# Performance work log

Measured on AMD Instinct MI355X. Metric: run time of the kernel, lower is better.

Reference implementation:

```python
import jax, jax.numpy as jnp
import numpy as np


def _layernorm(x, g, b, eps=1e-5):
    mu = jnp.mean(x, axis=-1, keepdims=True)
    xc = x - mu
    var = jnp.mean(xc * xc, axis=-1, keepdims=True)
    return xc * jax.lax.rsqrt(var + eps) * g + b


def _s5(u, Lambda_re, Lambda_im, B_re, B_im, C_re, C_im, Dskip, log_step):
    # Diagonal complex SSM with ZOH discretization (S5).
    Lam = Lambda_re + 1j * Lambda_im                       # (P,) complex64
    Lam_bar = jnp.exp(Lam * jnp.exp(log_step))             # (P,)
    B_bar = ((Lam_bar - 1.0) / Lam)[:, None] * (B_re + 1j * B_im)  # (P, D)
    Bu = jnp.einsum('bld,pd->blp', u.astype(jnp.complex64), B_bar)  # (B, L, P)
    A = jnp.broadcast_to(Lam_bar, Bu.shape)

    def combine(e1, e2):
        a1, b1 = e1
        a2, b2 = e2
        return a1 * a2, a2 * b1 + b2

    _, xs = jax.lax.associative_scan(combine, (A, Bu), axis=1)  # parallel scan over L
    y = 2.0 * jnp.real(jnp.einsum('blp,dp->bld', xs, C_re + 1j * C_im))
    return y + Dskip * u


def setup_inputs() -> dict:
    key = jax.random.key(0)
    ks = jax.random.split(key, 10)
    B, L, D, P = 4, 2048, 1024, 64
    F = int(D * 2.0)  # ff_mult = 2.0
    x = jax.random.normal(ks[0], (B, L, D), jnp.float32)
    ln1_g = jnp.ones((D,), jnp.float32)
    ln1_b = jnp.zeros((D,), jnp.float32)
    ln2_g = jnp.ones((D,), jnp.float32)
    ln2_b = jnp.zeros((D,), jnp.float32)
    Lambda_re = -(0.5 + jax.random.uniform(ks[1], (P,), jnp.float32))  # stable poles
    Lambda_im = jnp.pi * jnp.arange(P, dtype=jnp.float32)              # HiPPO-like spread
    B_re = jax.random.normal(ks[2], (P, D), jnp.float32) / np.float32(np.sqrt(D))
    B_im = jax.random.normal(ks[3], (P, D), jnp.float32) / np.float32(np.sqrt(D))
    C_re = jax.random.normal(ks[4], (D, P), jnp.float32) / np.float32(np.sqrt(P))
    C_im = jax.random.normal(ks[5], (D, P), jnp.float32) / np.float32(np.sqrt(P))
    Dskip = jax.random.normal(ks[6], (D,), jnp.float32)
    dt_min, dt_max = 1e-3, 1e-1
    log_step = (np.float32(np.log(dt_min))
                + jax.random.uniform(ks[7], (P,), jnp.float32)
                * np.float32(np.log(dt_max) - np.log(dt_min)))
    W_enc = jax.random.normal(ks[8], (2 * F, D), jnp.float32) / np.float32(np.sqrt(D))
    W_dec = jax.random.normal(ks[9], (D, F), jnp.float32) / np.float32(np.sqrt(F))
    return dict(x=x, ln1_g=ln1_g, ln1_b=ln1_b, ln2_g=ln2_g, ln2_b=ln2_b,
                Lambda_re=Lambda_re, Lambda_im=Lambda_im, B_re=B_re, B_im=B_im,
                C_re=C_re, C_im=C_im, Dskip=Dskip, log_step=log_step,
                W_enc=W_enc, W_dec=W_dec)


def reference(x, ln1_g, ln1_b, ln2_g, ln2_b, Lambda_re, Lambda_im, B_re, B_im,
              C_re, C_im, Dskip, log_step, W_enc, W_dec):
    # S5Block: pre-LN -> S5 -> GELU -> residual (dropout = identity in eval)
    fx = _layernorm(x, ln1_g, ln1_b)
    h = jax.nn.gelu(_s5(fx, Lambda_re, Lambda_im, B_re, B_im, C_re, C_im, Dskip, log_step),
                    approximate=False) + fx
    # pre-LN GEGLU feed-forward -> residual
    fx2 = _layernorm(h, ln2_g, ln2_b)
    e = fx2 @ W_enc.T                      # (B, L, 2F)
    a, gate = jnp.split(e, 2, axis=-1)
    e = a * jax.nn.gelu(gate, approximate=False)
    return e @ W_dec.T + fx2
```

## Files before the change

### kernel.cpp

```cpp
#include <hip/hip_runtime.h>
#include <hip/hip_bf16.h>
#include <math.h>

typedef unsigned short u16;
typedef __bf16 v8bf __attribute__((ext_vector_type(8)));
typedef float f32x4 __attribute__((ext_vector_type(4)));
typedef float f32x16 __attribute__((ext_vector_type(16)));

__device__ __forceinline__ float us2f(u16 h) {
    union { unsigned int u; float f; } v; v.u = ((unsigned int)h) << 16; return v.f;
}
__device__ __forceinline__ u16 f2us(float f) {
    union { float f; unsigned int u; } v; v.f = f;
    unsigned int r = v.u + 0x7fffu + ((v.u >> 16) & 1u);
    return (u16)(r >> 16);
}
__device__ __forceinline__ float gelu_f(float x) {
    return 0.5f * x * (1.0f + erff(x * 0.70710678118654752f));
}
__device__ __forceinline__ void gload_lds16(const u16* g, u16* l) {
    auto gp = reinterpret_cast<const __attribute__((address_space(1))) unsigned int*>(
        (uintptr_t)g);
    auto lp = reinterpret_cast<__attribute__((address_space(3))) unsigned int*>(
        (uintptr_t)l);
    __builtin_amdgcn_global_load_lds(gp, lp, 16, 0, 0);
}

__global__ __launch_bounds__(256) void prepall_kernel(
    const float* __restrict__ Wenc, u16* __restrict__ WeB,
    const float* __restrict__ Wdec, u16* __restrict__ WdB,
    const float* __restrict__ Lre, const float* __restrict__ Lim,
    const float* __restrict__ lstep,
    const float* __restrict__ Bre, const float* __restrict__ Bim,
    const float* __restrict__ Cre, const float* __restrict__ Cim,
    u16* __restrict__ Bbar, u16* __restrict__ C2)
{
    const int b = blockIdx.x, tid = threadIdx.x;
    if (b < 3072) {
        const float* in = (b < 2048) ? Wenc : Wdec;
        u16* outp = (b < 2048) ? WeB : WdB;
        const int i = (b < 2048 ? b : b - 2048) * 2048 + tid * 8;
        float4 a = *reinterpret_cast<const float4*>(in + i);
        float4 c = *reinterpret_cast<const float4*>(in + i + 4);
        u16 o[8] = { f2us(a.x), f2us(a.y), f2us(a.z), f2us(a.w),
                     f2us(c.x), f2us(c.y), f2us(c.z), f2us(c.w) };
        *reinterpret_cast<uint4*>(outp + i) = *reinterpret_cast<uint4*>(o);
        return;
    }
    const int idx = (b - 3072) * 256 + tid;
    if (idx < 65536) {
        const int p = idx >> 10, d = idx & 1023;
        const float lr = Lre[p], li = Lim[p];
        const float dt = expf(lstep[p]);
        const float er = expf(lr * dt);
        const float ar = er * cosf(li * dt), ai = er * sinf(li * dt);
        const float nr = ar - 1.0f, ni = ai;
        const float den = lr * lr + li * li;
        const float cr = (nr * lr + ni * li) / den;
        const float ci = (ni * lr - nr * li) / den;
        const float br = Bre[idx], bi = Bim[idx];
        Bbar[p * 1024 + d]        = f2us(cr * br - ci * bi);
        Bbar[(64 + p) * 1024 + d] = f2us(cr * bi + ci * br);
    } else {
        const int i = idx - 65536;
        const int d = i >> 6, p = i & 63;
        C2[d * 128 + p]      = f2us( 2.0f * Cre[i]);
        C2[d * 128 + 64 + p] = f2us(-2.0f * Cim[i]);
    }
}

template<typename TIN>
__global__ __launch_bounds__(256) void ln_kernel(const TIN* __restrict__ in,
                                                 const float* __restrict__ g,
                                                 const float* __restrict__ b,
                                                 u16* __restrict__ out)
{
    const int row = blockIdx.x, tid = threadIdx.x;
    const size_t base = (size_t)row * 1024 + tid * 4;
    float x0, x1, x2, x3;
    if constexpr (sizeof(TIN) == 4) {
        float4 v = *reinterpret_cast<const float4*>(in + base);
        x0 = v.x; x1 = v.y; x2 = v.z; x3 = v.w;
    } else {
        ushort4 v = *reinterpret_cast<const ushort4*>((const u16*)in + base);
        x0 = us2f(v.x); x1 = us2f(v.y); x2 = us2f(v.z); x3 = us2f(v.w);
    }
    float s = x0 + x1 + x2 + x3;
    float q = x0*x0 + x1*x1 + x2*x2 + x3*x3;
    #pragma unroll
    for (int o = 32; o; o >>= 1) { s += __shfl_down(s, o); q += __shfl_down(q, o); }
    __shared__ float red[8];
    if ((tid & 63) == 0) { red[tid >> 6] = s; red[4 + (tid >> 6)] = q; }
    __syncthreads();
    s = red[0] + red[1] + red[2] + red[3];
    q = red[4] + red[5] + red[6] + red[7];
    const float mu = s * (1.0f / 1024.0f);
    const float rs = rsqrtf(q * (1.0f / 1024.0f) - mu * mu + 1e-5f);
    float4 gv = *reinterpret_cast<const float4*>(g + tid * 4);
    float4 bv = *reinterpret_cast<const float4*>(b + tid * 4);
    ushort4 o4;
    o4.x = f2us((x0 - mu) * rs * gv.x + bv.x);
    o4.y = f2us((x1 - mu) * rs * gv.y + bv.y);
    o4.z = f2us((x2 - mu) * rs * gv.z + bv.z);
    o4.w = f2us((x3 - mu) * rs * gv.w + bv.w);
    *reinterpret_cast<ushort4*>(out + base) = o4;
}

__global__ __launch_bounds__(256) void scan_kernel(
    const float* __restrict__ Bu,
    const float* __restrict__ Lre, const float* __restrict__ Lim,
    const float* __restrict__ lstep,
    u16* __restrict__ A2)
{
    const int b = blockIdx.x >> 6;
    const int p = blockIdx.x & 63;
    const int t = threadIdx.x;
    const float lr = Lre[p], li = Lim[p];
    const float dt = expf(lstep[p]);
    const float er = expf(lr * dt);
    const float ar = er * cosf(li * dt), ai = er * sinf(li * dt);

    const size_t base = ((size_t)b * 2048 + t * 8) * 128;
    float xr[8], xi[8];
    float sr = 0.f, si = 0.f;
    #pragma unroll
    for (int i = 0; i < 8; ++i) {
        const float br = Bu[base + i * 128 + p];
        const float bi = Bu[base + i * 128 + 64 + p];
        const float nr = ar * sr - ai * si + br;
        const float ni = ar * si + ai * sr + bi;
        sr = nr; si = ni;
        xr[i] = sr; xi[i] = si;
    }
    float fr = ar, fi = ai;
    #pragma unroll
    for (int s = 0; s < 3; ++s) { const float t2 = fr*fr - fi*fi; fi = 2.f*fr*fi; fr = t2; }
    __shared__ float Er[256], Ei[256];
    Er[t] = sr; Ei[t] = si;
    __syncthreads();
    float vr = sr, vi = si;
    for (int off = 1; off < 256; off <<= 1) {
        float pr = 0.f, pi = 0.f;
        if (t >= off) { pr = Er[t - off]; pi = Ei[t - off]; }
        __syncthreads();
        vr += fr * pr - fi * pi;
        vi += fr * pi + fi * pr;
        Er[t] = vr; Ei[t] = vi;
        const float nf = fr*fr - fi*fi; fi = 2.f*fr*fi; fr = nf;
        __syncthreads();
    }
    float cr = 0.f, ci = 0.f;
    if (t > 0) { cr = Er[t - 1]; ci = Ei[t - 1]; }
    float gr = ar * cr - ai * ci, gi = ar * ci + ai * cr;
    #pragma unroll
    for (int i = 0; i < 8; ++i) {
        xr[i] += gr; xi[i] += gi;
        const float n2 = ar * gr - ai * gi; gi = ar * gi + ai * gr; gr = n2;
    }
    #pragma unroll
    for (int i = 0; i < 8; ++i) {
        const size_t m = (size_t)b * 2048 + t * 8 + i;
        A2[m * 128 + p]      = f2us(xr[i]);
        A2[m * 128 + 64 + p] = f2us(xi[i]);
    }
}

template<int BM, int BN>
__global__ __launch_bounds__(64) void gemm_small_kernel(
    const u16* __restrict__ A, const u16* __restrict__ B, float* __restrict__ Cout,
    const int N, const int K)
{
    __shared__ u16 lsA[BM * 32];
    __shared__ u16 lsB[BN * 32];
    const int tid = threadIdx.x;
    const int lane = tid & 63;
    const int m0 = blockIdx.y * BM, n0 = blockIdx.x * BN;
    f32x4 acc[4][4] = {};
    for (int k0 = 0; k0 < K; k0 += 32) {
        #pragma unroll
        for (int j = 0; j < 4; ++j) {
            const int s = j * 64 + tid;
            gload_lds16(A + (size_t)(m0 + (s >> 2)) * K + k0 + (s & 3) * 8,
                        lsA + (s - lane) * 8);
            gload_lds16(B + (size_t)(n0 + (s >> 2)) * K + k0 + (s & 3) * 8,
                        lsB + (s - lane) * 8);
        }
        __syncthreads();
        v8bf af[4], bfv[4];
        #pragma unroll
        for (int f = 0; f < 4; ++f)
            af[f] = *reinterpret_cast<const v8bf*>(
                lsA + (f * 16 + (lane & 15)) * 32 + (lane >> 4) * 8);
        #pragma unroll
        for (int f = 0; f < 4; ++f)
            bfv[f] = *reinterpret_cast<const v8bf*>(
                lsB + (f * 16 + (lane & 15)) * 32 + (lane >> 4) * 8);
        #pragma unroll
        for (int fm = 0; fm < 4; ++fm)
            #pragma unroll
            for (int fn = 0; fn < 4; ++fn)
                acc[fm][fn] = __builtin_amdgcn_mfma_f32_16x16x32_bf16(
                    af[fm], bfv[fn], acc[fm][fn], 0, 0, 0);
        __syncthreads();
    }
    #pragma unroll
    for (int fm = 0; fm < 4; ++fm)
    #pragma unroll
    for (int fn = 0; fn < 4; ++fn)
    #pragma unroll
    for (int i = 0; i < 4; ++i) {
        const int r = m0 + fm * 16 + (lane >> 4) * 4 + i;
        const int c = n0 + fn * 16 + (lane & 15);
        Cout[(size_t)r * N + c] = acc[fm][fn][i];
    }
}

#define BARM()   asm volatile("s_barrier" ::: "memory")
#define LGKM0()  asm volatile("s_waitcnt lgkmcnt(0)" ::: "memory")
#define VMK(n)   asm volatile("s_waitcnt vmcnt(" #n ")" ::: "memory")
#define PRIO1    __builtin_amdgcn_s_setprio(1)
#define PRIO0    __builtin_amdgcn_s_setprio(0)
#define MMA32(acc, a, b) \
    acc = __builtin_amdgcn_mfma_f32_32x32x16_bf16(a, b, acc, 0, 0, 0)

#define G_RA(af, kk, BI) { _Pragma("unroll") \
    for (int mf = 0; mf < 4; ++mf) \
        af[mf] = *reinterpret_cast<const v8bf*>(pA[kk] + mf * 2048 + (BI) * 16384); }
#define G_RB(kk, ag, BI) \
    (*reinterpret_cast<const v8bf*>(pB[kk] + (ag) * 8192 + (BI) * 16384))
#define G_ST(s, bi) do { \
    const int db_ = (((s) & 2) ? 32768 : 0) + (bi) * 16384 + (((s) & 1) ? 8192 : 0); \
    gload_lds16(pS[s][0], lds + db_ + (wid * 2 + 0) * 512); \
    gload_lds16(pS[s][1], lds + db_ + (wid * 2 + 1) * 512); \
    pS[s][0] += 64; pS[s][1] += 64; } while (0)
#define G_MM(kk) { _Pragma("unroll") \
    for (int mf = 0; mf < 4; ++mf) { \
        MMA32(accA[mf], af[mf], bA[kk]); MMA32(accG[mf], af[mf], bG[kk]); } }
#define G_TILE(BI, stA_, stB_) do { \
    v8bf af[4], bA[4], bG[4]; \
    G_RA(af, 0, BI); \
    _Pragma("unroll") for (int kk = 0; kk < 4; ++kk) { \
        bA[kk] = G_RB(kk, 0, BI); bG[kk] = G_RB(kk, 1, BI); } \
    if (stA_) G_ST(0, (BI) ^ 1); \
    PRIO1; G_MM(0); PRIO0; LGKM0(); BARM(); \
    G_RA(af, 1, BI); \
    if (stA_) G_ST(1, (BI) ^ 1); \
    PRIO1; G_MM(1); PRIO0; LGKM0(); BARM(); \
    G_RA(af, 2, BI); \
    if (stB_) G_ST(2, BI); \
    PRIO1; G_MM(2); PRIO0; LGKM0(); BARM(); \
    G_RA(af, 3, BI); \
    if (stB_) G_ST(3, BI); \
    PRIO1; G_MM(3); PRIO0; LGKM0(); \
    if (stB_) { VMK(4); } else { VMK(0); } \
    BARM(); } while (0)

template<int NBX>
__global__ __launch_bounds__(512, 2) void geglu_kernel(
    const u16* __restrict__ A, const u16* __restrict__ Bm, u16* __restrict__ Cout,
    const int K, const int NO, const int NT)
{
    __shared__ u16 lds[65536];
    const int tid = threadIdx.x, lane = tid & 63, wid = tid >> 6;
    const int wm = wid >> 2, wn = wid & 3;
    const int l31 = lane & 31, lh = lane >> 5, l7 = lane & 7;
    const int bid = blockIdx.x;
    const int chunk = (int)gridDim.x >> 3;
    const int swz = (bid & 7) * chunk + (bid >> 3);
    const int by = swz / NBX, bx = swz % NBX;
    const int m0 = by * 256, n0 = bx * 128;

    const int rl = lane >> 3;
    const int scol = ((lane & 7) ^ rl) * 8;
    const u16* pS[4][2];
    #pragma unroll
    for (int j = 0; j < 2; ++j) {
        const int rloc = (wid * 2 + j) * 8 + rl;
        pS[0][j] = A  + (size_t)(m0 + rloc)       * K + scol;
        pS[1][j] = A  + (size_t)(m0 + 128 + rloc) * K + scol;
        pS[2][j] = Bm + (size_t)(n0 + rloc)       * K + scol;
        pS[3][j] = Bm + (size_t)(NO + n0 + rloc)  * K + scol;
    }
    const u16* pA[4];
    const u16* pB[4];
    #pragma unroll
    for (int kk = 0; kk < 4; ++kk) {
        const int phys = ((kk * 2 + lh) ^ l7) * 8;
        pA[kk] = lds + (wm * 128 + l31) * 64 + phys;
        pB[kk] = lds + 32768 + (wn * 32 + l31) * 64 + phys;
    }

    f32x16 accA[4] = {};
    f32x16 accG[4] = {};

    #pragma unroll
    for (int t = 0; t < 2; ++t) { G_ST(0, t); G_ST(1, t); G_ST(2, t); G_ST(3, t); }
    VMK(0);
    BARM();

    const int NI = NT >> 1;
    for (int i = 0; i < NI; ++i) {
        const bool s1 = (i > 0);
        const bool s2 = (2 * i + 2 < NT);
        const bool s3 = (2 * i + 3 < NT);
        G_TILE(0, s1, s2);
        G_TILE(1, s2, s3);
    }

    #pragma unroll
    for (int mf = 0; mf < 4; ++mf)
    #pragma unroll
    for (int q = 0; q < 16; ++q) {
        const int r = m0 + wm * 128 + mf * 32 + (q & 3) + 8 * (q >> 2) + 4 * lh;
        const int c = n0 + wn * 32 + l31;
        Cout[(size_t)r * NO + c] = f2us(accA[mf][q] * gelu_f(accG[mf][q]));
    }
}

#define Q_RA2(af, k0_, BI) { _Pragma("unroll") \
    for (int mf = 0; mf < 2; ++mf) _Pragma("unroll") \
    for (int kq = 0; kq < 2; ++kq) \
        af[mf][kq] = *reinterpret_cast<const v8bf*>( \
            qA[(k0_) + kq] + mf * 2048 + (BI) * 8192); }
#define Q_ST(s, bi) do { \
    const int db_ = ((s) >= 4 ? 16384 : 0) + (bi) * 8192 + ((s) & 3) * 2048; \
    gload_lds16(qS[s], lds + db_ + wid * 512); qS[s] += 64; } while (0)
#define Q_TILE(BI, stA_, stB_) do { \
    v8bf af[2][2], bf[2][4]; \
    Q_RA2(af, 0, BI); \
    _Pragma("unroll") for (int cf = 0; cf < 2; ++cf) _Pragma("unroll") \
    for (int kk = 0; kk < 4; ++kk) \
        bf[cf][kk] = *reinterpret_cast<const v8bf*>( \
            qB[kk] + cf * 2048 + (BI) * 8192); \
    if (stA_) { Q_ST(0, (BI) ^ 1); Q_ST(1, (BI) ^ 1); Q_ST(2, (BI) ^ 1); Q_ST(3, (BI) ^ 1); } \
    PRIO1; \
    _Pragma("unroll") for (int mf = 0; mf < 2; ++mf) _Pragma("unroll") \
    for (int cf = 0; cf < 2; ++cf) { \
        MMA32(acc[mf][cf], af[mf][0], bf[cf][0]); \
        MMA32(acc[mf][cf], af[mf][1], bf[cf][1]); } \
    PRIO0; LGKM0(); BARM(); \
    Q_RA2(af, 2, BI); \
    if (stB_) { Q_ST(4, BI); Q_ST(5, BI); Q_ST(6, BI); Q_ST(7, BI); } \
    PRIO1; \
    _Pragma("unroll") for (int mf = 0; mf < 2; ++mf) _Pragma("unroll") \
    for (int cf = 0; cf < 2; ++cf) { \
        MMA32(acc[mf][cf], af[mf][0], bf[cf][2]); \
        MMA32(acc[mf][cf], af[mf][1], bf[cf][3]); } \
    PRIO0; LGKM0(); \
    if (stB_) { VMK(4); } else { VMK(0); } \
    BARM(); } while (0)

template<int EPI, int NBX>
__global__ __launch_bounds__(256, 2) void gemm4p_kernel(
    const u16* __restrict__ A, const u16* __restrict__ Bm, void* __restrict__ Cout,
    const int K, const int NO, const int NT,
    const u16* __restrict__ aux, const float* __restrict__ dskip)
{
    __shared__ u16 lds[32768];
    const int tid = threadIdx.x, lane = tid & 63, wid = tid >> 6;
    const int wm = wid >> 1, wn = wid & 1;
    const int l31 = lane & 31, lh = lane >> 5, l7 = lane & 7;
    const int bid = blockIdx.x;
    const int chunk = (int)gridDim.x >> 3;
    const int swz = (bid & 7) * chunk + (bid >> 3);
    const int by = swz / NBX, bx = swz % NBX;
    const int m0 = by * 128, n0 = bx * 128;

    const int rl = lane >> 3;
    const int scol = ((lane & 7) ^ rl) * 8;
    const u16* qS[8];
    #pragma unroll
    for (int s = 0; s < 4; ++s)
        qS[s] = A + (size_t)(m0 + s * 32 + wid * 8 + rl) * K + scol;
    #pragma unroll
    for (int s = 4; s < 8; ++s)
        qS[s] = Bm + (size_t)(n0 + (s - 4) * 32 + wid * 8 + rl) * K + scol;
    const u16* qA[4];
    const u16* qB[4];
    #pragma unroll
    for (int kk = 0; kk < 4; ++kk) {
        const int phys = ((kk * 2 + lh) ^ l7) * 8;
        qA[kk] = lds + (wm * 64 + l31) * 64 + phys;
        qB[kk] = lds + 16384 + (wn * 64 + l31) * 64 + phys;
    }

    f32x16 acc[2][2] = {};

    #pragma unroll
    for (int t = 0; t < 2; ++t) {
        Q_ST(0, t); Q_ST(1, t); Q_ST(2, t); Q_ST(3, t);
        Q_ST(4, t); Q_ST(5, t); Q_ST(6, t); Q_ST(7, t);
    }
    VMK(0);
    BARM();

    const int NI = NT >> 1;
    for (int i = 0; i < NI; ++i) {
        const bool s1 = (i > 0);
        const bool s2 = (2 * i + 2 < NT);
        const bool s3 = (2 * i + 3 < NT);
        Q_TILE(0, s1, s2);
        Q_TILE(1, s2, s3);
    }

    #pragma unroll
    for (int mf = 0; mf < 2; ++mf)
    #pragma unroll
    for (int cf = 0; cf < 2; ++cf)
    #pragma unroll
    for (int q = 0; q < 16; ++q) {
        const int r = m0 + wm * 64 + mf * 32 + (q & 3) + 8 * (q >> 2) + 4 * lh;
        const int c = n0 + wn * 64 + cf * 32 + l31;
        const size_t o = (size_t)r * NO + c;
        const float v = acc[mf][cf][q];
        if constexpr (EPI == 1) {
            const float u = us2f(aux[o]);
            const float t2 = v + dskip[c] * u;
            ((u16*)Cout)[o] = f2us(gelu_f(t2) + u);
        } else {
            ((float*)Cout)[o] = v + us2f(aux[o]);
        }
    }
}

static constexpr size_t OFF_FX  = 0;
static constexpr size_t OFF_BU  = 16777216;
static constexpr size_t OFF_A2  = 20971520;
static constexpr size_t OFF_E2  = 0;
static constexpr size_t OFF_FX2 = 33554432;
static constexpr size_t OFF_BB  = 50331648;
static constexpr size_t OFF_C2  = 50593792;
static constexpr size_t OFF_WE  = 50855936;
static constexpr size_t OFF_WD  = 59244544;

extern "C" void kernel_launch(void* const* d_in, const int* in_sizes, int n_in,
                              void* d_out, int out_size, void* d_ws, size_t ws_size,
                              hipStream_t stream) {
    const float* x    = (const float*)d_in[0];
    const float* l1g  = (const float*)d_in[1];
    const float* l1b  = (const float*)d_in[2];
    const float* l2g  = (const float*)d_in[3];
    const float* l2b  = (const float*)d_in[4];
    const float* Lre  = (const float*)d_in[5];
    const float* Lim  = (const float*)d_in[6];
    const float* Bre  = (const float*)d_in[7];
    const float* Bim  = (const float*)d_in[8];
    const float* Cre  = (const float*)d_in[9];
    const float* Cim  = (const float*)d_in[10];
    const float* Dsk  = (const float*)d_in[11];
    const float* lst  = (const float*)d_in[12];
    const float* Wenc = (const float*)d_in[13];
    const float* Wdec = (const float*)d_in[14];
    float* out = (float*)d_out;

    char* ws = (char*)d_ws;
    u16*   fx   = (u16*)(ws + OFF_FX);
    float* Bu   = (float*)(ws + OFF_BU);
    u16*   A2   = (u16*)(ws + OFF_A2);
    u16*   e2   = (u16*)(ws + OFF_E2);
    u16*   fx2  = (u16*)(ws + OFF_FX2);
    u16*   Bbar = (u16*)(ws + OFF_BB);
    u16*   C2   = (u16*)(ws + OFF_C2);
    u16*   WeB  = (u16*)(ws + OFF_WE);
    u16*   WdB  = (u16*)(ws + OFF_WD);
    u16*   h    = (u16*)d_out;

    ln_kernel<float><<<8192, 256, 0, stream>>>(x, l1g, l1b, fx);
    prepall_kernel<<<3584, 256, 0, stream>>>(Wenc, WeB, Wdec, WdB,
                                             Lre, Lim, lst, Bre, Bim, Cre, Cim,
                                             Bbar, C2);
    gemm_small_kernel<64, 64><<<dim3(2, 128), 64, 0, stream>>>(
        fx, Bbar, Bu, 128, 1024);
    scan_kernel<<<256, 256, 0, stream>>>(Bu, Lre, Lim, lst, A2);
    gemm4p_kernel<1, 8><<<512, 256, 0, stream>>>(
        A2, C2, h, 128, 1024, 2, fx, Dsk);
    ln_kernel<u16><<<8192, 256, 0, stream>>>(h, l2g, l2b, fx2);
    geglu_kernel<16><<<512, 512, 0, stream>>>(fx2, WeB, e2, 1024, 2048, 16);
    gemm4p_kernel<3, 8><<<512, 256, 0, stream>>>(
        e2, WdB, out, 2048, 1024, 32, fx2, nullptr);

    (void)in_sizes; (void)n_in; (void)out_size; (void)ws_size;
}
```

Before: 223.4 us.

## Triple-buffer A tiles in GEGLU GEMM and fuse LN1 into prep kernel

The GEGLU GEMM now keeps three A-tile LDS buffers and two B-tile buffers. Loads are issued two K-tiles ahead and waited on with a looser vmcnt, so global-to-LDS traffic overlaps more MFMA work. The K-tile count becomes a template parameter so the loop fully unrolls. LDS per block grows to 160KB. The first LayerNorm is merged into the weight/SSM prep kernel, saving one launch. That fused LayerNorm computes variance in a single pass as E[x²]−mu², which is slightly less numerically robust.

```diff
diff --git a/kernel.cpp b/kernel.cpp
--- a/kernel.cpp
+++ b/kernel.cpp
@@ -26,7 +26,9 @@
     __builtin_amdgcn_global_load_lds(gp, lp, 16, 0, 0);
 }
 
-__global__ __launch_bounds__(256) void prepall_kernel(
+__global__ __launch_bounds__(256) void pre_kernel(
+    const float* __restrict__ x, const float* __restrict__ l1g,
+    const float* __restrict__ l1b, u16* __restrict__ fx,
     const float* __restrict__ Wenc, u16* __restrict__ WeB,
     const float* __restrict__ Wdec, u16* __restrict__ WdB,
     const float* __restrict__ Lre, const float* __restrict__ Lim,
@@ -35,7 +37,33 @@
     const float* __restrict__ Cre, const float* __restrict__ Cim,
     u16* __restrict__ Bbar, u16* __restrict__ C2)
 {
-    const int b = blockIdx.x, tid = threadIdx.x;
+    const int blk = blockIdx.x, tid = threadIdx.x;
+    if (blk < 8192) {
+        const size_t base = (size_t)blk * 1024 + tid * 4;
+        float4 v = *reinterpret_cast<const float4*>(x + base);
+        float x0 = v.x, x1 = v.y, x2 = v.z, x3 = v.w;
+        float s = x0 + x1 + x2 + x3;
+        float q = x0*x0 + x1*x1 + x2*x2 + x3*x3;
+        #pragma unroll
+        for (int o = 32; o; o >>= 1) { s += __shfl_down(s, o); q += __shfl_down(q, o); }
+        __shared__ float red[8];
+        if ((tid & 63) == 0) { red[tid >> 6] = s; red[4 + (tid >> 6)] = q; }
+        __syncthreads();
+        s = red[0] + red[1] + red[2] + red[3];
+        q = red[4] + red[5] + red[6] + red[7];
+        const float mu = s * (1.0f / 1024.0f);
+        const float rs = rsqrtf(q * (1.0f / 1024.0f) - mu * mu + 1e-5f);
+        float4 gv = *reinterpret_cast<const float4*>(l1g + tid * 4);
+        float4 bv = *reinterpret_cast<const float4*>(l1b + tid * 4);
+        ushort4 o4;
+        o4.x = f2us((x0 - mu) * rs * gv.x + bv.x);
+        o4.y = f2us((x1 - mu) * rs * gv.y + bv.y);
+        o4.z = f2us((x2 - mu) * rs * gv.z + bv.z);
+        o4.w = f2us((x3 - mu) * rs * gv.w + bv.w);
+        *reinterpret_cast<ushort4*>(fx + base) = o4;
+        return;
+    }
+    const int b = blk - 8192;
     if (b < 3072) {
         const float* in = (b < 2048) ? Wenc : Wdec;
         u16* outp = (b < 2048) ? WeB : WdB;
@@ -223,44 +251,30 @@
 #define MMA32(acc, a, b) \
     acc = __builtin_amdgcn_mfma_f32_32x32x16_bf16(a, b, acc, 0, 0, 0)
 
-#define G_RA(af, kk, BI) { _Pragma("unroll") \
+#define G_RA(af, kk, AI) { _Pragma("unroll") \
     for (int mf = 0; mf < 4; ++mf) \
-        af[mf] = *reinterpret_cast<const v8bf*>(pA[kk] + mf * 2048 + (BI) * 16384); }
+        af[mf] = *reinterpret_cast<const v8bf*>( \
+            pA[kk] + (AI) * 16384 + mf * 2048); }
 #define G_RB(kk, ag, BI) \
-    (*reinterpret_cast<const v8bf*>(pB[kk] + (ag) * 8192 + (BI) * 16384))
-#define G_ST(s, bi) do { \
-    const int db_ = (((s) & 2) ? 32768 : 0) + (bi) * 16384 + (((s) & 1) ? 8192 : 0); \
-    gload_lds16(pS[s][0], lds + db_ + (wid * 2 + 0) * 512); \
-    gload_lds16(pS[s][1], lds + db_ + (wid * 2 + 1) * 512); \
+    (*reinterpret_cast<const v8bf*>(pB[kk] + (BI) * 16384 + (ag) * 8192))
+#define G_STA(s, ai) do { \
+    gload_lds16(pS[s][0], lds + (ai) * 16384 + (s) * 8192 + (wid * 2 + 0) * 512); \
+    gload_lds16(pS[s][1], lds + (ai) * 16384 + (s) * 8192 + (wid * 2 + 1) * 512); \
+    pS[s][0] += 64; pS[s][1] += 64; } while (0)
+#define G_STB(s, bi) do { \
+    gload_lds16(pS[s][0], lds + 49152 + (bi) * 16384 + ((s) - 2) * 8192 + (wid * 2 + 0) * 512); \
+    gload_lds16(pS[s][1], lds + 49152 + (bi) * 16384 + ((s) - 2) * 8192 + (wid * 2 + 1) * 512); \
     pS[s][0] += 64; pS[s][1] += 64; } while (0)
 #define G_MM(kk) { _Pragma("unroll") \
     for (int mf = 0; mf < 4; ++mf) { \
         MMA32(accA[mf], af[mf], bA[kk]); MMA32(accG[mf], af[mf], bG[kk]); } }
-#define G_TILE(BI, stA_, stB_) do { \
-    v8bf af[4], bA[4], bG[4]; \
-    G_RA(af, 0, BI); \
-    _Pragma("unroll") for (int kk = 0; kk < 4; ++kk) { \
-        bA[kk] = G_RB(kk, 0, BI); bG[kk] = G_RB(kk, 1, BI); } \
-    if (stA_) G_ST(0, (BI) ^ 1); \
-    PRIO1; G_MM(0); PRIO0; LGKM0(); BARM(); \
-    G_RA(af, 1, BI); \
-    if (stA_) G_ST(1, (BI) ^ 1); \
-    PRIO1; G_MM(1); PRIO0; LGKM0(); BARM(); \
-    G_RA(af, 2, BI); \
-    if (stB_) G_ST(2, BI); \
-    PRIO1; G_MM(2); PRIO0; LGKM0(); BARM(); \
-    G_RA(af, 3, BI); \
-    if (stB_) G_ST(3, BI); \
-    PRIO1; G_MM(3); PRIO0; LGKM0(); \
-    if (stB_) { VMK(4); } else { VMK(0); } \
-    BARM(); } while (0)
-
-template<int NBX>
+
+template<int NBX, int NT>
 __global__ __launch_bounds__(512, 2) void geglu_kernel(
     const u16* __restrict__ A, const u16* __restrict__ Bm, u16* __restrict__ Cout,
-    const int K, const int NO, const int NT)
+    const int K, const int NO)
 {
-    __shared__ u16 lds[65536];
+    __shared__ u16 lds[81920];
     const int tid = threadIdx.x, lane = tid & 63, wid = tid >> 6;
     const int wm = wid >> 2, wn = wid & 3;
     const int l31 = lane & 31, lh = lane >> 5, l7 = lane & 7;
@@ -287,24 +301,42 @@
     for (int kk = 0; kk < 4; ++kk) {
         const int phys = ((kk * 2 + lh) ^ l7) * 8;
         pA[kk] = lds + (wm * 128 + l31) * 64 + phys;
-        pB[kk] = lds + 32768 + (wn * 32 + l31) * 64 + phys;
+        pB[kk] = lds + 49152 + (wn * 32 + l31) * 64 + phys;
     }
 
     f32x16 accA[4] = {};
     f32x16 accG[4] = {};
 
-    #pragma unroll
-    for (int t = 0; t < 2; ++t) { G_ST(0, t); G_ST(1, t); G_ST(2, t); G_ST(3, t); }
-    VMK(0);
+    G_STA(0, 0); G_STA(1, 0);
+    G_STB(2, 0); G_STB(3, 0);
+    G_STA(0, 1); G_STA(1, 1);
+    G_STB(2, 1); G_STB(3, 1);
+    VMK(8);
     BARM();
 
-    const int NI = NT >> 1;
-    for (int i = 0; i < NI; ++i) {
-        const bool s1 = (i > 0);
-        const bool s2 = (2 * i + 2 < NT);
-        const bool s3 = (2 * i + 3 < NT);
-        G_TILE(0, s1, s2);
-        G_TILE(1, s2, s3);
+    #pragma unroll
+    for (int t = 0; t < NT; ++t) {
+        const int AI = t % 3, AN = (t + 2) % 3, BI = t & 1;
+        const bool st = (t + 2 < NT);
+        v8bf af[4], bA[4], bG[4];
+        G_RA(af, 0, AI);
+        #pragma unroll
+        for (int kk = 0; kk < 4; ++kk) {
+            bA[kk] = G_RB(kk, 0, BI); bG[kk] = G_RB(kk, 1, BI);
+        }
+        if (st) G_STA(0, AN);
+        PRIO1; G_MM(0); PRIO0; LGKM0(); BARM();
+        G_RA(af, 1, AI);
+        if (st) G_STA(1, AN);
+        PRIO1; G_MM(1); PRIO0; LGKM0(); BARM();
+        G_RA(af, 2, AI);
+        if (st) G_STB(2, BI);
+        PRIO1; G_MM(2); PRIO0; LGKM0(); BARM();
+        G_RA(af, 3, AI);
+        if (st) G_STB(3, BI);
+        PRIO1; G_MM(3); PRIO0; LGKM0();
+        if (st) { VMK(8); } else { VMK(0); }
+        BARM();
     }
 
     #pragma unroll
@@ -465,17 +497,17 @@
     u16*   WdB  = (u16*)(ws + OFF_WD);
     u16*   h    = (u16*)d_out;
 
-    ln_kernel<float><<<8192, 256, 0, stream>>>(x, l1g, l1b, fx);
-    prepall_kernel<<<3584, 256, 0, stream>>>(Wenc, WeB, Wdec, WdB,
-                                             Lre, Lim, lst, Bre, Bim, Cre, Cim,
-                                             Bbar, C2);
+    pre_kernel<<<11776, 256, 0, stream>>>(x, l1g, l1b, fx,
+                                          Wenc, WeB, Wdec, WdB,
+                                          Lre, Lim, lst, Bre, Bim, Cre, Cim,
+                                          Bbar, C2);
     gemm_small_kernel<64, 64><<<dim3(2, 128), 64, 0, stream>>>(
         fx, Bbar, Bu, 128, 1024);
     scan_kernel<<<256, 256, 0, stream>>>(Bu, Lre, Lim, lst, A2);
     gemm4p_kernel<1, 8><<<512, 256, 0, stream>>>(
         A2, C2, h, 128, 1024, 2, fx, Dsk);
     ln_kernel<u16><<<8192, 256, 0, stream>>>(h, l2g, l2b, fx2);
-    geglu_kernel<16><<<512, 512, 0, stream>>>(fx2, WeB, e2, 1024, 2048, 16);
+    geglu_kernel<16, 16><<<512, 512, 0, stream>>>(fx2, WeB, e2, 1024, 2048);
     gemm4p_kernel<3, 8><<<512, 256, 0, stream>>>(
         e2, WdB, out, 2048, 1024, 32, fx2, nullptr);
 
```

After: 221.5 us. No clear change (-0.8%).
